# Optimization experiments

Measured on AMD Instinct MI355X. Metric: run time of the kernel, lower is better.

## Reference

```python
import jax, jax.numpy as jnp
import numpy as np

FRAME_T = 8
NUM_K = 10


def _masked_att(att, temp):
    # att: [B, H, P, P] -> softmax over groups of size P//FRAME_T, top-k threshold mask
    B, H, P, _ = att.shape
    D = P // FRAME_T
    a = att.reshape(B, H, P, FRAME_T, D)
    a = jax.nn.softmax(a / temp, axis=-1)
    # k-th largest value per row as threshold (torch.topk values are sorted desc)
    margin = jax.lax.top_k(a, NUM_K)[0][..., -1]  # [B,H,P,FRAME_T]
    a = a * (a >= margin[..., None])
    return a  # [B,H,P,FRAME_T,D]


def setup_inputs() -> dict:
    key = jax.random.key(0)
    k1, k2, k3, k4 = jax.random.split(key, 4)
    B, H, P, hd = 4, 12, 1568, 64
    return {
        "att_s": jax.random.normal(k1, (B, H, P, P), dtype=jnp.float32),
        "att_t": jax.random.normal(k2, (B, H, P, P), dtype=jnp.float32),
        "v_s": jax.random.normal(k3, (B, H, P, hd), dtype=jnp.float32),
        "v_t": jax.random.normal(k4, (B, H, P, hd), dtype=jnp.float32),
    }


def reference(att_s, att_t, v_s, v_t):
    temp = jnp.float32(1.0)
    B, H, P, _ = att_t.shape
    H_s = att_s.shape[1]
    h_dim = v_t.shape[-1]
    D = P // FRAME_T

    a_s = _masked_att(att_s, temp)  # [B,Hs,P,T,D]
    a_t = _masked_att(att_t, temp)  # [B,H,P,T,D]

    vt = v_t.reshape(B, H, D, FRAME_T, h_dim)
    vs = v_s.reshape(B, H_s, D, FRAME_T, h_dim)

    norm_s = a_s.sum(-1)  # [B,Hs,P,T]
    norm_t = a_t.sum(-1)

    o_s = jnp.einsum('bhptd,bhdte->bhpte', a_s, vs) / norm_s[..., None]
    o_t = jnp.einsum('bhptd,bhdte->bhpte', a_t, vt) / norm_t[..., None]

    loss = jnp.mean((o_s - o_t) ** 2)
    return loss
```

## Files before the change

### kernel.cpp

```cpp
#include <hip/hip_runtime.h>
#include <hip/hip_bf16.h>

#define PP 1568
#define TT 8
#define DD 196
#define HD 64
#define NBH 48
#define NROW (NBH*PP*TT)
#define RPW 32
#define WPB 2
#define NWAVE (NROW/RPW)
#define NBLK5 (NWAVE/WPB)
#define NXCD 8
#define CPX (NBLK5/NXCD)
#define NPART NWAVE
#define NRED1 ((NPART+255)/256)
#define SUB (8*DD*4)
#define VSLAB (DD*TT*HD)
#define WPBH 392
#define KMASK 0xFFFFFF00u
#define NEG_INF (-3.0e38f)

typedef float f4 __attribute__((ext_vector_type(4)));
typedef unsigned u4v __attribute__((ext_vector_type(4)));

__device__ __forceinline__ float readlane_f(float v, int l) {
    return __int_as_float(__builtin_amdgcn_readlane(__float_as_int(v), l));
}

__device__ __forceinline__ float wave_sum_u(float v) {
#define STEPS(ctrl) { float t_ = __int_as_float(__builtin_amdgcn_update_dpp( \
        0, __float_as_int(v), ctrl, 0xF, 0xF, true)); v += t_; }
    STEPS(0x111) STEPS(0x112) STEPS(0x114) STEPS(0x118) STEPS(0x142) STEPS(0x143)
#undef STEPS
    return readlane_f(v, 63);
}

__device__ __forceinline__ float kval(float k) {
    return __uint_as_float(__float_as_uint(k) & KMASK);
}

__device__ __forceinline__ void gload_lds(const void* g, void* l) {
    __builtin_amdgcn_global_load_lds(
        (const __attribute__((address_space(1))) unsigned*)g,
        (__attribute__((address_space(3))) unsigned*)l, 16, 0, 0);
}

struct K6  { float k0,k1,k2,k3,k4,k5; };
struct K10 { float k0,k1,k2,k3,k4,k5,k6,k7,k8,k9; };
struct MR  { K10 f; float mx; };

#define PUTK6(Q,X,D) { \
  unsigned cu_=(__float_as_uint(X)&KMASK)|(unsigned)(D); \
  float c_=__uint_as_float(cu_); \
  float n0_=fmaxf(Q.k0,c_); \
  float n1_=__builtin_amdgcn_fmed3f(Q.k0,Q.k1,c_); \
  float n2_=__builtin_amdgcn_fmed3f(Q.k1,Q.k2,c_); \
  float n3_=__builtin_amdgcn_fmed3f(Q.k2,Q.k3,c_); \
  float n4_=__builtin_amdgcn_fmed3f(Q.k3,Q.k4,c_); \
  float n5_=__builtin_amdgcn_fmed3f(Q.k4,Q.k5,c_); \
  Q.k0=n0_; Q.k1=n1_; Q.k2=n2_; Q.k3=n3_; Q.k4=n4_; Q.k5=n5_; }
#define PUT4K6(Q,V,D0) PUTK6(Q,(V).x,(D0)) PUTK6(Q,(V).y,(D0)+1) \
                       PUTK6(Q,(V).z,(D0)+2) PUTK6(Q,(V).w,(D0)+3)

__device__ __forceinline__ K6 chain_rows(const char* stg, int a, int b8) {
    K6 q = {NEG_INF,NEG_INF,NEG_INF,NEG_INF,NEG_INF,NEG_INF};
    const char* rb = stg + a*784 + b8*16;
    f4 v;
    v = *(const f4*)(rb);       PUT4K6(q, v, b8*4)
    v = *(const f4*)(rb+128);   PUT4K6(q, v, b8*4+32)
    v = *(const f4*)(rb+256);   PUT4K6(q, v, b8*4+64)
    v = *(const f4*)(rb+384);   PUT4K6(q, v, b8*4+96)
    v = *(const f4*)(rb+512);   PUT4K6(q, v, b8*4+128)
    v = *(const f4*)(rb+640);   PUT4K6(q, v, b8*4+160)
    if (b8 == 7) { f4 w = *(const f4*)(stg + a*784 + 768); PUT4K6(q, w, 192) }
    return q;
}

#define FSWZ(x, pat) __int_as_float(__builtin_amdgcn_ds_swizzle(__float_as_int(x), pat))
__device__ __forceinline__ K6 kshuf8_6(K6 a) {
    K6 r;
    r.k0=FSWZ(a.k0,0x201F); r.k1=FSWZ(a.k1,0x201F); r.k2=FSWZ(a.k2,0x201F);
    r.k3=FSWZ(a.k3,0x201F); r.k4=FSWZ(a.k4,0x201F); r.k5=FSWZ(a.k5,0x201F);
    return r;
}
__device__ __forceinline__ K10 kshuf16(K10 a) {
    K10 r;
    r.k0=FSWZ(a.k0,0x401F); r.k1=FSWZ(a.k1,0x401F); r.k2=FSWZ(a.k2,0x401F);
    r.k3=FSWZ(a.k3,0x401F); r.k4=FSWZ(a.k4,0x401F); r.k5=FSWZ(a.k5,0x401F);
    r.k6=FSWZ(a.k6,0x401F); r.k7=FSWZ(a.k7,0x401F); r.k8=FSWZ(a.k8,0x401F);
    r.k9=FSWZ(a.k9,0x401F);
    return r;
}
__device__ __forceinline__ float fbp(int bpx, float x) {
    return __int_as_float(__builtin_amdgcn_ds_bpermute(bpx, __float_as_int(x)));
}
__device__ __forceinline__ K10 kbp32(K10 a, int bpx) {
    K10 r;
    r.k0=fbp(bpx,a.k0); r.k1=fbp(bpx,a.k1); r.k2=fbp(bpx,a.k2);
    r.k3=fbp(bpx,a.k3); r.k4=fbp(bpx,a.k4); r.k5=fbp(bpx,a.k5);
    r.k6=fbp(bpx,a.k6); r.k7=fbp(bpx,a.k7); r.k8=fbp(bpx,a.k8);
    r.k9=fbp(bpx,a.k9);
    return r;
}

__device__ __forceinline__ K10 kmrg66(K6 A, K6 B) {
    float p00=fminf(A.k0,B.k0);
    float p01=fminf(A.k0,B.k1), p10=fminf(A.k1,B.k0);
    float p02=fminf(A.k0,B.k2), p11=fminf(A.k1,B.k1), p20=fminf(A.k2,B.k0);
    float p03=fminf(A.k0,B.k3), p12=fminf(A.k1,B.k2), p21=fminf(A.k2,B.k1), p30=fminf(A.k3,B.k0);
    float p04=fminf(A.k0,B.k4), p13=fminf(A.k1,B.k3), p22=fminf(A.k2,B.k2), p31=fminf(A.k3,B.k1), p40=fminf(A.k4,B.k0);
    float p05=fminf(A.k0,B.k5), p14=fminf(A.k1,B.k4), p23=fminf(A.k2,B.k3), p32=fminf(A.k3,B.k2), p41=fminf(A.k4,B.k1), p50=fminf(A.k5,B.k0);
    float p15=fminf(A.k1,B.k5), p24=fminf(A.k2,B.k4), p33=fminf(A.k3,B.k3), p42=fminf(A.k4,B.k2), p51=fminf(A.k5,B.k1);
    float p25=fminf(A.k2,B.k5), p34=fminf(A.k3,B.k4), p43=fminf(A.k4,B.k3), p52=fminf(A.k5,B.k2);
    float p35=fminf(A.k3,B.k5), p44=fminf(A.k4,B.k4), p53=fminf(A.k5,B.k3);
    K10 M;
    M.k0=fmaxf(A.k0,B.k0);
    M.k1=fmaxf(fmaxf(A.k1,B.k1),p00);
    M.k2=fmaxf(fmaxf(A.k2,B.k2),fmaxf(p01,p10));
    M.k3=fmaxf(fmaxf(A.k3,B.k3),fmaxf(p02,fmaxf(p11,p20)));
    M.k4=fmaxf(fmaxf(A.k4,B.k4),fmaxf(fmaxf(p03,p12),fmaxf(p21,p30)));
    M.k5=fmaxf(fmaxf(A.k5,B.k5),fmaxf(fmaxf(p04,p13),fmaxf(p22,fmaxf(p31,p40))));
    M.k6=fmaxf(fmaxf(p05,p14),fmaxf(fmaxf(p23,p32),fmaxf(p41,p50)));
    M.k7=fmaxf(fmaxf(p15,p24),fmaxf(p33,fmaxf(p42,p51)));
    M.k8=fmaxf(fmaxf(p25,p34),fmaxf(p43,p52));
    M.k9=fmaxf(p35,fmaxf(p44,p53));
    return M;
}

__device__ __forceinline__ K10 kmrg(K10 A, K10 B) {
    float p00=fminf(A.k0,B.k0);
    float p01=fminf(A.k0,B.k1), p10=fminf(A.k1,B.k0);
    float p02=fminf(A.k0,B.k2), p11=fminf(A.k1,B.k1), p20=fminf(A.k2,B.k0);
    float p03=fminf(A.k0,B.k3), p12=fminf(A.k1,B.k2), p21=fminf(A.k2,B.k1), p30=fminf(A.k3,B.k0);
    float p04=fminf(A.k0,B.k4), p13=fminf(A.k1,B.k3), p22=fminf(A.k2,B.k2), p31=fminf(A.k3,B.k1), p40=fminf(A.k4,B.k0);
    float p05=fminf(A.k0,B.k5), p14=fminf(A.k1,B.k4), p23=fminf(A.k2,B.k3), p32=fminf(A.k3,B.k2), p41=fminf(A.k4,B.k1), p50=fminf(A.k5,B.k0);
    float p06=fminf(A.k0,B.k6), p15=fminf(A.k1,B.k5), p24=fminf(A.k2,B.k4), p33=fminf(A.k3,B.k3), p42=fminf(A.k4,B.k2), p51=fminf(A.k5,B.k1), p60=fminf(A.k6,B.k0);
    float p07=fminf(A.k0,B.k7), p16=fminf(A.k1,B.k6), p25=fminf(A.k2,B.k5), p34=fminf(A.k3,B.k4), p43=fminf(A.k4,B.k3), p52=fminf(A.k5,B.k2), p61=fminf(A.k6,B.k1), p70=fminf(A.k7,B.k0);
    float p08=fminf(A.k0,B.k8), p17=fminf(A.k1,B.k7), p26=fminf(A.k2,B.k6), p35=fminf(A.k3,B.k5), p44=fminf(A.k4,B.k4), p53=fminf(A.k5,B.k3), p62=fminf(A.k6,B.k2), p71=fminf(A.k7,B.k1), p80=fminf(A.k8,B.k0);
    K10 M;
    M.k0=fmaxf(A.k0,B.k0);
    M.k1=fmaxf(fmaxf(A.k1,B.k1),p00);
    M.k2=fmaxf(fmaxf(A.k2,B.k2),fmaxf(p01,p10));
    M.k3=fmaxf(fmaxf(A.k3,B.k3),fmaxf(p02,fmaxf(p11,p20)));
    M.k4=fmaxf(fmaxf(A.k4,B.k4),fmaxf(fmaxf(p03,p12),fmaxf(p21,p30)));
    M.k5=fmaxf(fmaxf(A.k5,B.k5),fmaxf(fmaxf(p04,p13),fmaxf(p22,fmaxf(p31,p40))));
    M.k6=fmaxf(fmaxf(A.k6,B.k6),fmaxf(fmaxf(p05,p14),fmaxf(fmaxf(p23,p32),fmaxf(p41,p50))));
    M.k7=fmaxf(fmaxf(A.k7,B.k7),fmaxf(fmaxf(fmaxf(p06,p15),fmaxf(p24,p33)),fmaxf(fmaxf(p42,p51),p60)));
    M.k8=fmaxf(fmaxf(A.k8,B.k8),fmaxf(fmaxf(fmaxf(p07,p16),fmaxf(p25,p34)),fmaxf(fmaxf(p43,p52),fmaxf(p61,p70))));
    M.k9=fmaxf(fmaxf(A.k9,B.k9),fmaxf(fmaxf(fmaxf(p08,p17),fmaxf(p26,p35)),fmaxf(fmaxf(p44,p53),fmaxf(fmaxf(p62,p71),p80))));
    return M;
}

__device__ __forceinline__ MR merge_all(K6 q, int bpx) {
    K10 m = kmrg66(q, kshuf8_6(q));
    K10 n = kmrg(m, kshuf16(m));
    K10 r = kbp32(n, bpx);
    MR out;
    out.mx = fmaxf(n.k0, r.k0);
    out.f.k0=fmaxf(n.k0,r.k9); out.f.k1=fmaxf(n.k1,r.k8); out.f.k2=fmaxf(n.k2,r.k7);
    out.f.k3=fmaxf(n.k3,r.k6); out.f.k4=fmaxf(n.k4,r.k5); out.f.k5=fmaxf(n.k5,r.k4);
    out.f.k6=fmaxf(n.k6,r.k3); out.f.k7=fmaxf(n.k7,r.k2); out.f.k8=fmaxf(n.k8,r.k1);
    out.f.k9=fmaxf(n.k9,r.k0);
    return out;
}

#define STAGE(SRC) { const char* s_=(SRC); \
    gload_lds(s_ +         (size_t)lane*16, stg); \
    gload_lds(s_ + 1024 +  (size_t)lane*16, stg+1024); \
    gload_lds(s_ + 2048 +  (size_t)lane*16, stg+2048); \
    gload_lds(s_ + 3072 +  (size_t)lane*16, stg+3072); \
    gload_lds(s_ + 4096 +  (size_t)lane*16, stg+4096); \
    gload_lds(s_ + 5120 +  (size_t)lane*16, stg+5120); \
    if (lane < 8) gload_lds(s_ + 6144 + (size_t)lane*16, stg+6144); }
#define WAITV asm volatile("s_waitcnt vmcnt(0)" ::: "memory");

#define PKW(F,K) ((__float_as_uint(F)&KMASK)|(__float_as_uint(K)&0xFFu))

__global__ __launch_bounds__(128) void vtop_main(
        const float* __restrict__ att_s, const float* __restrict__ att_t,
        const float* __restrict__ v_s,   const float* __restrict__ v_t,
        float* __restrict__ partial) {
    __shared__ f4  stgv[WPB][SUB/16];
    __shared__ u4v wbuf[WPB][5][RPW];

    int tid  = threadIdx.x;
    int wid  = tid >> 6;
    int lane = tid & 63;
    char* stg = (char*)&stgv[wid][0];
    int a = lane & 7, b8 = lane >> 3;
    int bpx = (lane ^ 32) << 2;

    int blk = (blockIdx.x % NXCD) * CPX + blockIdx.x / NXCD;
    int gwave = blk * WPB + wid;
    int bh = gwave / WPBH;

    const char* baseS = (const char*)att_s + (size_t)gwave * (RPW*DD*4);
    const char* baseT = (const char*)att_t + (size_t)gwave * (RPW*DD*4);

    STAGE(baseS)

#pragma unroll 1
    for (int s = 0; s < 4; ++s) {
        int row = (s << 3) | (lane & 7);
        WAITV
        K6 qS = chain_rows(stg, a, b8);
        STAGE(baseT + s*SUB)
        {
            MR mS = merge_all(qS, bpx);
            K10 fS = mS.f;
            float CS = kval(mS.mx);
            float wS0=__expf(kval(fS.k0)-CS), wS1=__expf(kval(fS.k1)-CS),
                  wS2=__expf(kval(fS.k2)-CS), wS3=__expf(kval(fS.k3)-CS),
                  wS4=__expf(kval(fS.k4)-CS), wS5=__expf(kval(fS.k5)-CS),
                  wS6=__expf(kval(fS.k6)-CS), wS7=__expf(kval(fS.k7)-CS),
                  wS8=__expf(kval(fS.k8)-CS), wS9=__expf(kval(fS.k9)-CS);
            float wsS = (((wS0+wS1)+(wS2+wS3))+((wS4+wS5)+(wS6+wS7)))+(wS8+wS9);
            float invS = __builtin_amdgcn_rcpf(wsS);
            if (lane < 8) {
                u4v w;
                w.x=PKW(wS0*invS,fS.k0); w.y=PKW(wS1*invS,fS.k1);
                w.z=PKW(wS2*invS,fS.k2); w.w=PKW(wS3*invS,fS.k3);
                wbuf[wid][0][row]=w;
                w.x=PKW(wS4*invS,fS.k4); w.y=PKW(wS5*invS,fS.k5);
                w.z=PKW(wS6*invS,fS.k6); w.w=PKW(wS7*invS,fS.k7);
                wbuf[wid][1][row]=w;
                unsigned* h = (unsigned*)&wbuf[wid][2][row];
                h[0]=PKW(wS8*invS,fS.k8); h[1]=PKW(wS9*invS,fS.k9);
            }
        }

        WAITV
        K6 qT = chain_rows(stg, a, b8);
        if (s < 3) STAGE(baseS + (s+1)*SUB)
        {
            MR mT = merge_all(qT, bpx);
            K10 fT = mT.f;
            float CT = kval(mT.mx);
            float wT0=__expf(kval(fT.k0)-CT), wT1=__expf(kval(fT.k1)-CT),
                  wT2=__expf(kval(fT.k2)-CT), wT3=__expf(kval(fT.k3)-CT),
                  wT4=__expf(kval(fT.k4)-CT), wT5=__expf(kval(fT.k5)-CT),
                  wT6=__expf(kval(fT.k6)-CT), wT7=__expf(kval(fT.k7)-CT),
                  wT8=__expf(kval(fT.k8)-CT), wT9=__expf(kval(fT.k9)-CT);
            float wsT = (((wT0+wT1)+(wT2+wT3))+((wT4+wT5)+(wT6+wT7)))+(wT8+wT9);
            float invT = -__builtin_amdgcn_rcpf(wsT);
            if (lane < 8) {
                unsigned* h = (unsigned*)&wbuf[wid][2][row];
                h[2]=PKW(wT0*invT,fT.k0); h[3]=PKW(wT1*invT,fT.k1);
                u4v w;
                w.x=PKW(wT2*invT,fT.k2); w.y=PKW(wT3*invT,fT.k3);
                w.z=PKW(wT4*invT,fT.k4); w.w=PKW(wT5*invT,fT.k5);
                wbuf[wid][3][row]=w;
                w.x=PKW(wT6*invT,fT.k6); w.y=PKW(wT7*invT,fT.k7);
                w.z=PKW(wT8*invT,fT.k8); w.w=PKW(wT9*invT,fT.k9);
                wbuf[wid][4][row]=w;
            }
        }
    }

    const float* vSb = v_s + (size_t)bh * VSLAB;
    const float* vTb = v_t + (size_t)bh * VSLAB;
    unsigned ul = (unsigned)lane;
    float lacc = 0.f;
#pragma unroll 1
    for (int k = 0; k < RPW; ++k) {
        unsigned t64 = ((unsigned)(k & 7) << 6);
        const float* vSk = vSb + t64;
        const float* vTk = vTb + t64;
        u4v w0v=wbuf[wid][0][k], w1v=wbuf[wid][1][k], w2v=wbuf[wid][2][k],
            w3v=wbuf[wid][3][k], w4v=wbuf[wid][4][k];
        float d0=0.f, d1=0.f, d2=0.f, d3=0.f;
#define TRM(U, VB, ACC) { unsigned pk_=(unsigned)__builtin_amdgcn_readfirstlane((int)(U)); \
        float wf_ = __uint_as_float(pk_ & KMASK); \
        ACC = fmaf(wf_, VB[((pk_ & 0xFFu) << 9) + ul], ACC); }
        TRM(w0v.x, vSk, d0) TRM(w0v.y, vSk, d1) TRM(w0v.z, vSk, d2) TRM(w0v.w, vSk, d3)
        TRM(w1v.x, vSk, d0) TRM(w1v.y, vSk, d1) TRM(w1v.z, vSk, d2) TRM(w1v.w, vSk, d3)
        TRM(w2v.x, vSk, d0) TRM(w2v.y, vSk, d1)
        TRM(w2v.z, vTk, d2) TRM(w2v.w, vTk, d3)
        TRM(w3v.x, vTk, d0) TRM(w3v.y, vTk, d1) TRM(w3v.z, vTk, d2) TRM(w3v.w, vTk, d3)
        TRM(w4v.x, vTk, d0) TRM(w4v.y, vTk, d1) TRM(w4v.z, vTk, d2) TRM(w4v.w, vTk, d3)
#undef TRM
        float dsum = (d0 + d1) + (d2 + d3);
        lacc = fmaf(dsum, dsum, lacc);
    }

    float tot = wave_sum_u(lacc);
    if (lane == 0) partial[gwave] = tot;
}

__global__ __launch_bounds__(256) void vtop_reduce1(
        const float* __restrict__ partial, float* __restrict__ p2) {
    int i = blockIdx.x * 256 + threadIdx.x;
    float v = (i < NPART) ? partial[i] : 0.f;
    float wtot = wave_sum_u(v);
    __shared__ float sm[4];
    int lane = threadIdx.x & 63, wid = threadIdx.x >> 6;
    if (lane == 0) sm[wid] = wtot;
    __syncthreads();
    if (threadIdx.x == 0) p2[blockIdx.x] = (sm[0] + sm[1]) + (sm[2] + sm[3]);
}

__global__ __launch_bounds__(256) void vtop_reduce2(
        const float* __restrict__ p2, float* __restrict__ out) {
    __shared__ double smd[256];
    double a = 0.0;
    if (threadIdx.x < NRED1) a = (double)p2[threadIdx.x];
    smd[threadIdx.x] = a;
    __syncthreads();
    for (int s = 128; s > 0; s >>= 1) {
        if (threadIdx.x < s) smd[threadIdx.x] += smd[threadIdx.x + s];
        __syncthreads();
    }
    if (threadIdx.x == 0) {
        const double inv_n = 1.0 / ((double)NBH * PP * TT * HD);
        out[0] = (float)(smd[0] * inv_n);
    }
}

extern "C" void kernel_launch(void* const* d_in, const int* in_sizes, int n_in,
                              void* d_out, int out_size, void* d_ws, size_t ws_size,
                              hipStream_t stream) {
    const float* att_s = (const float*)d_in[0];
    const float* att_t = (const float*)d_in[1];
    const float* v_s   = (const float*)d_in[2];
    const float* v_t   = (const float*)d_in[3];
    float* out     = (float*)d_out;
    float* partial = (float*)d_ws;
    float* p2      = (float*)d_ws + NPART;

    vtop_main<<<NBLK5, 128, 0, stream>>>(att_s, att_t, v_s, v_t, partial);
    vtop_reduce1<<<NRED1, 256, 0, stream>>>(partial, p2);
    vtop_reduce2<<<1, 256, 0, stream>>>(p2, out);
}
```

Baseline: 308.3 us.

## Split fused kernel into top-k selection and V-product kernels via workspace

Splits the fused kernel into two. One kernel streams the attention rows, computes the packed top-k weights and indices, and writes them to a global workspace. A second kernel with 256-thread blocks reads those weights and does the gather-FMA against V to produce the per-wave partial sums. The intent is to separate the bandwidth-bound streaming phase from the gather phase so each can run with its own occupancy and block shape. The cost is an extra kernel launch plus a small global write and read of the packed weights, and the fused path remains only as a fallback when the workspace is too small.

```diff
diff --git a/kernel.cpp b/kernel.cpp
--- a/kernel.cpp
+++ b/kernel.cpp
@@ -13,6 +13,9 @@
 #define NBLK5 (NWAVE/WPB)
 #define NXCD 8
 #define CPX (NBLK5/NXCD)
+#define WPBP 4
+#define NBLK6 (NWAVE/WPBP)
+#define CPX6 (NBLK6/NXCD)
 #define NPART NWAVE
 #define NRED1 ((NPART+255)/256)
 #define SUB (8*DD*4)
@@ -20,9 +23,12 @@
 #define WPBH 392
 #define KMASK 0xFFFFFF00u
 #define NEG_INF (-3.0e38f)
+#define WQ_OFF 80000
+#define ROWB 80
 
 typedef float f4 __attribute__((ext_vector_type(4)));
 typedef unsigned u4v __attribute__((ext_vector_type(4)));
+typedef unsigned u2v __attribute__((ext_vector_type(2)));
 
 __device__ __forceinline__ float readlane_f(float v, int l) {
     return __int_as_float(__builtin_amdgcn_readlane(__float_as_int(v), l));
@@ -177,6 +183,127 @@
 
 #define PKW(F,K) ((__float_as_uint(F)&KMASK)|(__float_as_uint(K)&0xFFu))
 
+#define SBODY(EMIT10) { \
+    MR mS = merge_all(qS, bpx); \
+    K10 fS = mS.f; \
+    float CS = kval(mS.mx); \
+    float wS0=__expf(kval(fS.k0)-CS), wS1=__expf(kval(fS.k1)-CS), \
+          wS2=__expf(kval(fS.k2)-CS), wS3=__expf(kval(fS.k3)-CS), \
+          wS4=__expf(kval(fS.k4)-CS), wS5=__expf(kval(fS.k5)-CS), \
+          wS6=__expf(kval(fS.k6)-CS), wS7=__expf(kval(fS.k7)-CS), \
+          wS8=__expf(kval(fS.k8)-CS), wS9=__expf(kval(fS.k9)-CS); \
+    float wsS = (((wS0+wS1)+(wS2+wS3))+((wS4+wS5)+(wS6+wS7)))+(wS8+wS9); \
+    float invS = __builtin_amdgcn_rcpf(wsS); \
+    if (lane < 8) { EMIT10 } }
+#define TBODY(EMIT10) { \
+    MR mT = merge_all(qT, bpx); \
+    K10 fT = mT.f; \
+    float CT = kval(mT.mx); \
+    float wT0=__expf(kval(fT.k0)-CT), wT1=__expf(kval(fT.k1)-CT), \
+          wT2=__expf(kval(fT.k2)-CT), wT3=__expf(kval(fT.k3)-CT), \
+          wT4=__expf(kval(fT.k4)-CT), wT5=__expf(kval(fT.k5)-CT), \
+          wT6=__expf(kval(fT.k6)-CT), wT7=__expf(kval(fT.k7)-CT), \
+          wT8=__expf(kval(fT.k8)-CT), wT9=__expf(kval(fT.k9)-CT); \
+    float wsT = (((wT0+wT1)+(wT2+wT3))+((wT4+wT5)+(wT6+wT7)))+(wT8+wT9); \
+    float invT = -__builtin_amdgcn_rcpf(wsT); \
+    if (lane < 8) { EMIT10 } }
+
+__global__ __launch_bounds__(128) void vtop_sel(
+        const float* __restrict__ att_s, const float* __restrict__ att_t,
+        char* __restrict__ wq) {
+    __shared__ f4 stgv[WPB][SUB/16];
+
+    int tid  = threadIdx.x;
+    int wid  = tid >> 6;
+    int lane = tid & 63;
+    char* stg = (char*)&stgv[wid][0];
+    int a = lane & 7, b8 = lane >> 3;
+    int bpx = (lane ^ 32) << 2;
+
+    int blk = (blockIdx.x % NXCD) * CPX + blockIdx.x / NXCD;
+    int gwave = blk * WPB + wid;
+
+    const char* baseS = (const char*)att_s + (size_t)gwave * (RPW*DD*4);
+    const char* baseT = (const char*)att_t + (size_t)gwave * (RPW*DD*4);
+    char* wqw = wq + (size_t)gwave * (RPW*ROWB);
+
+    STAGE(baseS)
+
+#pragma unroll 1
+    for (int s = 0; s < 4; ++s) {
+        char* rp = wqw + (size_t)((s << 3) | (lane & 7)) * ROWB;
+        WAITV
+        K6 qS = chain_rows(stg, a, b8);
+        STAGE(baseT + s*SUB)
+        SBODY(
+            u4v w;
+            w.x=PKW(wS0*invS,fS.k0); w.y=PKW(wS1*invS,fS.k1);
+            w.z=PKW(wS2*invS,fS.k2); w.w=PKW(wS3*invS,fS.k3);
+            *(u4v*)(rp) = w;
+            w.x=PKW(wS4*invS,fS.k4); w.y=PKW(wS5*invS,fS.k5);
+            w.z=PKW(wS6*invS,fS.k6); w.w=PKW(wS7*invS,fS.k7);
+            *(u4v*)(rp+16) = w;
+            u2v h; h.x=PKW(wS8*invS,fS.k8); h.y=PKW(wS9*invS,fS.k9);
+            *(u2v*)(rp+32) = h;
+        )
+        WAITV
+        K6 qT = chain_rows(stg, a, b8);
+        if (s < 3) STAGE(baseS + (s+1)*SUB)
+        TBODY(
+            u2v h; h.x=PKW(wT0*invT,fT.k0); h.y=PKW(wT1*invT,fT.k1);
+            *(u2v*)(rp+40) = h;
+            u4v w;
+            w.x=PKW(wT2*invT,fT.k2); w.y=PKW(wT3*invT,fT.k3);
+            w.z=PKW(wT4*invT,fT.k4); w.w=PKW(wT5*invT,fT.k5);
+            *(u4v*)(rp+48) = w;
+            w.x=PKW(wT6*invT,fT.k6); w.y=PKW(wT7*invT,fT.k7);
+            w.z=PKW(wT8*invT,fT.k8); w.w=PKW(wT9*invT,fT.k9);
+            *(u4v*)(rp+64) = w;
+        )
+    }
+}
+
+__global__ __launch_bounds__(256) void vtop_prod(
+        const float* __restrict__ v_s, const float* __restrict__ v_t,
+        const char* __restrict__ wq, float* __restrict__ partial) {
+    int tid  = threadIdx.x;
+    int wid  = tid >> 6;
+    int lane = tid & 63;
+
+    int blk = (blockIdx.x % NXCD) * CPX6 + blockIdx.x / NXCD;
+    int gwave = blk * WPBP + wid;
+    int bh = gwave / WPBH;
+
+    const u4v* wqw = (const u4v*)(wq + (size_t)gwave * (RPW*ROWB));
+    const float* vSb = v_s + (size_t)bh * VSLAB;
+    const float* vTb = v_t + (size_t)bh * VSLAB;
+    unsigned ul = (unsigned)lane;
+    float lacc = 0.f;
+#pragma unroll 1
+    for (int k = 0; k < RPW; ++k) {
+        unsigned t64 = ((unsigned)(k & 7) << 6);
+        const float* vSk = vSb + t64;
+        const float* vTk = vTb + t64;
+        u4v w0v=wqw[k*5+0], w1v=wqw[k*5+1], w2v=wqw[k*5+2],
+            w3v=wqw[k*5+3], w4v=wqw[k*5+4];
+        float d0=0.f, d1=0.f, d2=0.f, d3=0.f;
+#define TRM(U, VB, ACC) { unsigned pk_=(unsigned)__builtin_amdgcn_readfirstlane((int)(U)); \
+        float wf_ = __uint_as_float(pk_ & KMASK); \
+        ACC = fmaf(wf_, VB[((pk_ & 0xFFu) << 9) + ul], ACC); }
+        TRM(w0v.x, vSk, d0) TRM(w0v.y, vSk, d1) TRM(w0v.z, vSk, d2) TRM(w0v.w, vSk, d3)
+        TRM(w1v.x, vSk, d0) TRM(w1v.y, vSk, d1) TRM(w1v.z, vSk, d2) TRM(w1v.w, vSk, d3)
+        TRM(w2v.x, vSk, d0) TRM(w2v.y, vSk, d1)
+        TRM(w2v.z, vTk, d2) TRM(w2v.w, vTk, d3)
+        TRM(w3v.x, vTk, d0) TRM(w3v.y, vTk, d1) TRM(w3v.z, vTk, d2) TRM(w3v.w, vTk, d3)
+        TRM(w4v.x, vTk, d0) TRM(w4v.y, vTk, d1) TRM(w4v.z, vTk, d2) TRM(w4v.w, vTk, d3)
+#undef TRM
+        float dsum = (d0 + d1) + (d2 + d3);
+        lacc = fmaf(dsum, dsum, lacc);
+    }
+    float tot = wave_sum_u(lacc);
+    if (lane == 0) partial[gwave] = tot;
+}
+
 __global__ __launch_bounds__(128) void vtop_main(
         const float* __restrict__ att_s, const float* __restrict__ att_t,
         const float* __restrict__ v_s,   const float* __restrict__ v_t,
@@ -206,56 +333,31 @@
         WAITV
         K6 qS = chain_rows(stg, a, b8);
         STAGE(baseT + s*SUB)
-        {
-            MR mS = merge_all(qS, bpx);
-            K10 fS = mS.f;
-            float CS = kval(mS.mx);
-            float wS0=__expf(kval(fS.k0)-CS), wS1=__expf(kval(fS.k1)-CS),
-                  wS2=__expf(kval(fS.k2)-CS), wS3=__expf(kval(fS.k3)-CS),
-                  wS4=__expf(kval(fS.k4)-CS), wS5=__expf(kval(fS.k5)-CS),
-                  wS6=__expf(kval(fS.k6)-CS), wS7=__expf(kval(fS.k7)-CS),
-                  wS8=__expf(kval(fS.k8)-CS), wS9=__expf(kval(fS.k9)-CS);
-            float wsS = (((wS0+wS1)+(wS2+wS3))+((wS4+wS5)+(wS6+wS7)))+(wS8+wS9);
-            float invS = __builtin_amdgcn_rcpf(wsS);
-            if (lane < 8) {
-                u4v w;
-                w.x=PKW(wS0*invS,fS.k0); w.y=PKW(wS1*invS,fS.k1);
-                w.z=PKW(wS2*invS,fS.k2); w.w=PKW(wS3*invS,fS.k3);
-                wbuf[wid][0][row]=w;
-                w.x=PKW(wS4*invS,fS.k4); w.y=PKW(wS5*invS,fS.k5);
-                w.z=PKW(wS6*invS,fS.k6); w.w=PKW(wS7*invS,fS.k7);
-                wbuf[wid][1][row]=w;
-                unsigned* h = (unsigned*)&wbuf[wid][2][row];
-                h[0]=PKW(wS8*invS,fS.k8); h[1]=PKW(wS9*invS,fS.k9);
-            }
-        }
-
+        SBODY(
+            u4v w;
+            w.x=PKW(wS0*invS,fS.k0); w.y=PKW(wS1*invS,fS.k1);
+            w.z=PKW(wS2*invS,fS.k2); w.w=PKW(wS3*invS,fS.k3);
+            wbuf[wid][0][row]=w;
+            w.x=PKW(wS4*invS,fS.k4); w.y=PKW(wS5*invS,fS.k5);
+            w.z=PKW(wS6*invS,fS.k6); w.w=PKW(wS7*invS,fS.k7);
+            wbuf[wid][1][row]=w;
+            unsigned* h = (unsigned*)&wbuf[wid][2][row];
+            h[0]=PKW(wS8*invS,fS.k8); h[1]=PKW(wS9*invS,fS.k9);
+        )
         WAITV
         K6 qT = chain_rows(stg, a, b8);
         if (s < 3) STAGE(baseS + (s+1)*SUB)
-        {
-            MR mT = merge_all(qT, bpx);
-            K10 fT = mT.f;
-            float CT = kval(mT.mx);
-            float wT0=__expf(kval(fT.k0)-CT), wT1=__expf(kval(fT.k1)-CT),
-                  wT2=__expf(kval(fT.k2)-CT), wT3=__expf(kval(fT.k3)-CT),
-                  wT4=__expf(kval(fT.k4)-CT), wT5=__expf(kval(fT.k5)-CT),
-                  wT6=__expf(kval(fT.k6)-CT), wT7=__expf(kval(fT.k7)-CT),
-                  wT8=__expf(kval(fT.k8)-CT), wT9=__expf(kval(fT.k9)-CT);
-            float wsT = (((wT0+wT1)+(wT2+wT3))+((wT4+wT5)+(wT6+wT7)))+(wT8+wT9);
-            float invT = -__builtin_amdgcn_rcpf(wsT);
-            if (lane < 8) {
-                unsigned* h = (unsigned*)&wbuf[wid][2][row];
-                h[2]=PKW(wT0*invT,fT.k0); h[3]=PKW(wT1*invT,fT.k1);
-                u4v w;
-                w.x=PKW(wT2*invT,fT.k2); w.y=PKW(wT3*invT,fT.k3);
-                w.z=PKW(wT4*invT,fT.k4); w.w=PKW(wT5*invT,fT.k5);
-                wbuf[wid][3][row]=w;
-                w.x=PKW(wT6*invT,fT.k6); w.y=PKW(wT7*invT,fT.k7);
-                w.z=PKW(wT8*invT,fT.k8); w.w=PKW(wT9*invT,fT.k9);
-                wbuf[wid][4][row]=w;
-            }
-        }
+        TBODY(
+            unsigned* h = (unsigned*)&wbuf[wid][2][row];
+            h[2]=PKW(wT0*invT,fT.k0); h[3]=PKW(wT1*invT,fT.k1);
+            u4v w;
+            w.x=PKW(wT2*invT,fT.k2); w.y=PKW(wT3*invT,fT.k3);
+            w.z=PKW(wT4*invT,fT.k4); w.w=PKW(wT5*invT,fT.k5);
+            wbuf[wid][3][row]=w;
+            w.x=PKW(wT6*invT,fT.k6); w.y=PKW(wT7*invT,fT.k7);
+            w.z=PKW(wT8*invT,fT.k8); w.w=PKW(wT9*invT,fT.k9);
+            wbuf[wid][4][row]=w;
+        )
     }
 
     const float* vSb = v_s + (size_t)bh * VSLAB;
@@ -328,7 +430,14 @@
     float* partial = (float*)d_ws;
     float* p2      = (float*)d_ws + NPART;
 
-    vtop_main<<<NBLK5, 128, 0, stream>>>(att_s, att_t, v_s, v_t, partial);
+    size_t need = (size_t)WQ_OFF + (size_t)NWAVE * (RPW*ROWB);
+    if (ws_size >= need) {
+        char* wq = (char*)d_ws + WQ_OFF;
+        vtop_sel <<<NBLK5, 128, 0, stream>>>(att_s, att_t, wq);
+        vtop_prod<<<NBLK6, 256, 0, stream>>>(v_s, v_t, wq, partial);
+    } else {
+        vtop_main<<<NBLK5, 128, 0, stream>>>(att_s, att_t, v_s, v_t, partial);
+    }
     vtop_reduce1<<<NRED1, 256, 0, stream>>>(partial, p2);
     vtop_reduce2<<<1, 256, 0, stream>>>(p2, out);
 }
```

New measurement: 423.1 us. 1.37x slower.
